# Optimization experiments

Hardware: AMD Instinct MI355X
Metric: run time of the kernel (lower is better)

## Reference

```python
import jax, jax.numpy as jnp
import numpy as np
import math

B, N, IN_DIM, OUT_DIM, H = 8, 1024, 256, 256, 8
D_K = OUT_DIM // H


def setup_inputs() -> dict:
    key = jax.random.key(0)
    ks = jax.random.split(key, 12)
    s_in = 1.0 / math.sqrt(IN_DIM)
    s_out = 1.0 / math.sqrt(OUT_DIM)
    return {
        "X": jax.random.normal(ks[0], (B, N, IN_DIM), jnp.float32),
        "A": jax.random.randint(ks[1], (B, N, N), 0, 2, jnp.int32),
        "D": jax.random.uniform(ks[2], (B, N, N), jnp.float32),
        "W_q": jax.random.uniform(ks[3], (IN_DIM, OUT_DIM), jnp.float32, -s_in, s_in),
        "b_q": jax.random.uniform(ks[4], (OUT_DIM,), jnp.float32, -s_in, s_in),
        "W_k": jax.random.uniform(ks[5], (IN_DIM, OUT_DIM), jnp.float32, -s_in, s_in),
        "b_k": jax.random.uniform(ks[6], (OUT_DIM,), jnp.float32, -s_in, s_in),
        "W_v": jax.random.uniform(ks[7], (IN_DIM, OUT_DIM), jnp.float32, -s_in, s_in),
        "b_v": jax.random.uniform(ks[8], (OUT_DIM,), jnp.float32, -s_in, s_in),
        "W_o": jax.random.uniform(ks[9], (OUT_DIM, OUT_DIM), jnp.float32, -s_out, s_out),
        "b_o": jax.random.uniform(ks[10], (OUT_DIM,), jnp.float32, -s_out, s_out),
        "dist_scale": jnp.array(1.0, jnp.float32),
    }


def reference(X, A, D, W_q, b_q, W_k, b_k, W_v, b_v, W_o, b_o, dist_scale):
    b, n, _ = X.shape
    # Projections -> [B, H, N, d_k]
    Q = (X @ W_q + b_q).reshape(b, n, H, D_K).transpose(0, 2, 1, 3)
    K = (X @ W_k + b_k).reshape(b, n, H, D_K).transpose(0, 2, 1, 3)
    V = (X @ W_v + b_v).reshape(b, n, H, D_K).transpose(0, 2, 1, 3)
    scores = jnp.einsum("bhqd,bhkd->bhqk", Q, K) / jnp.sqrt(jnp.float32(D_K))
    scores = scores - dist_scale * D[:, None, :, :]
    scores = jnp.where(A[:, None, :, :] <= 0, jnp.float32(-1e9), scores)
    attn = jax.nn.softmax(scores, axis=-1)  # dropout is identity in eval mode
    out = jnp.einsum("bhqk,bhkd->bhqd", attn, V)
    out = out.transpose(0, 2, 1, 3).reshape(b, n, H * D_K)
    return out @ W_o + b_o
```

## Files before the change

### kernel.cpp

```cpp
#include <hip/hip_runtime.h>


typedef _Float16 f16x8 __attribute__((ext_vector_type(8)));
typedef __fp16 h16x2 __attribute__((ext_vector_type(2)));
typedef float f32x4 __attribute__((ext_vector_type(4)));
typedef int i32x4 __attribute__((ext_vector_type(4)));
typedef unsigned short u16x8 __attribute__((ext_vector_type(8)));

#define DEV static __device__ __forceinline__

#define LOG2E 1.4426950408889634f
#define QSCALE 0.2550351062f

DEV unsigned short f2h(float f) {
  _Float16 h = (_Float16)f;
  unsigned short u;
  __builtin_memcpy(&u, &h, 2);
  return u;
}

DEV f32x4 mfma16h(f16x8 a, f16x8 b, f32x4 c) {
  return __builtin_amdgcn_mfma_f32_16x16x32_f16(a, b, c, 0, 0, 0);
}

DEV f16x8 ldfragh(const unsigned short* p) {
  return *reinterpret_cast<const f16x8*>(p);
}

__global__ __launch_bounds__(256) void k_prep(
    const float* __restrict__ X, const int* __restrict__ A,
    const float* __restrict__ D, const float* __restrict__ dscale,
    const float* __restrict__ Wq, const float* __restrict__ Wk,
    const float* __restrict__ Wv, const float* __restrict__ Wo,
    unsigned short* __restrict__ Xh, unsigned short* __restrict__ Wt,
    unsigned short* __restrict__ Bias) {
  const int tid = blockIdx.x * 256 + threadIdx.x;
  const int NB4 = (8 * 1024 * 1024) / 4;
  const int NX4 = (8192 * 256) / 4;
  if (tid < NB4) {
    const i32x4 a4 = reinterpret_cast<const i32x4*>(A)[tid];
    const f32x4 d4 = reinterpret_cast<const f32x4*>(D)[tid];
    const float c = -dscale[0] * LOG2E;
    ushort4 o;
    unsigned short* op = (unsigned short*)&o;
    #pragma unroll
    for (int i = 0; i < 4; ++i)
      op[i] = f2h(a4[i] <= 0 ? -60000.0f : c * d4[i]);
    reinterpret_cast<ushort4*>(Bias)[tid] = o;
  } else if (tid < NB4 + NX4) {
    const int t = tid - NB4;
    float4 v = reinterpret_cast<const float4*>(X)[t];
    union { h16x2 h2[2]; ushort4 u; } o;
    o.h2[0] = __builtin_amdgcn_cvt_pkrtz(v.x, v.y);
    o.h2[1] = __builtin_amdgcn_cvt_pkrtz(v.z, v.w);
    reinterpret_cast<ushort4*>(Xh)[t] = o.u;
  } else {
    int t = tid - NB4 - NX4;
    int mat = t >> 16;
    int e = t & 65535;
    int n = e >> 8, k = e & 255;
    const float* W = (mat == 0) ? Wq : (mat == 1) ? Wk : (mat == 2) ? Wv : Wo;
    Wt[t] = f2h(W[k * 256 + n]);
  }
}

__global__ __launch_bounds__(256, 2) void k_qkv(
    const unsigned short* __restrict__ Xh, const unsigned short* __restrict__ Wt,
    const float* __restrict__ bq, const float* __restrict__ bk,
    const float* __restrict__ bv,
    unsigned short* __restrict__ Qb, unsigned short* __restrict__ Kb,
    unsigned short* __restrict__ Vt) {
  const int lane = threadIdx.x & 63;
  const int w = threadIdx.x >> 6;
  const int lr = lane & 15, lg = lane >> 4;
  const int mat = blockIdx.y >> 2;
  const int nloc = (blockIdx.y & 3) * 64 + w * 16;
  const int mbase = blockIdx.x << 8;

  const unsigned short* Wm = Wt + mat * 65536;
  const float* bias = (mat == 0) ? bq : (mat == 1) ? bk : bv;

  f16x8 bfr[8];
  #pragma unroll
  for (int ks = 0; ks < 8; ++ks)
    bfr[ks] = ldfragh(Wm + (nloc + lr) * 256 + ks * 32 + lg * 8);
  const float bb = bias[nloc + lr];
  const int cm = nloc + lr;
  const int hh = cm >> 5, d = cm & 31;

  for (int mt = 0; mt < 16; ++mt) {
    const int m0 = mbase + mt * 16;
    f16x8 a[8];
    #pragma unroll
    for (int ks = 0; ks < 8; ++ks)
      a[ks] = ldfragh(Xh + (m0 + lr) * 256 + ks * 32 + lg * 8);
    f32x4 acc = {0.f, 0.f, 0.f, 0.f};
    #pragma unroll
    for (int ks = 0; ks < 8; ++ks)
      acc = mfma16h(a[ks], bfr[ks], acc);

    if (mat == 2) {
      union { h16x2 h2[2]; ushort4 u; } vv;
      vv.h2[0] = __builtin_amdgcn_cvt_pkrtz(acc[0] + bb, acc[1] + bb);
      vv.h2[1] = __builtin_amdgcn_cvt_pkrtz(acc[2] + bb, acc[3] + bb);
      const int row = m0 + lg * 4;
      const int bidx = row >> 10, nn = row & 1023;
      *reinterpret_cast<ushort4*>(&Vt[(((bidx * 8 + hh) * 32) + d) * 1024 + nn]) = vv.u;
    } else if (mat == 0) {
      #pragma unroll
      for (int i = 0; i < 4; ++i) {
        const int row = m0 + lg * 4 + i;
        const int bidx = row >> 10, nn = row & 1023;
        Qb[(((bidx * 8 + hh) * 1024) + nn) * 32 + d] = f2h((acc[i] + bb) * QSCALE);
      }
    } else {
      #pragma unroll
      for (int i = 0; i < 4; ++i) {
        const int row = m0 + lg * 4 + i;
        const int bidx = row >> 10, nn = row & 1023;
        Kb[(((bidx * 8 + hh) * 1024) + nn) * 32 + d] = f2h(acc[i] + bb);
      }
    }
  }
}

__global__ __launch_bounds__(512, 2) void k_attn(
    const unsigned short* __restrict__ Qb, const unsigned short* __restrict__ Kb,
    const unsigned short* __restrict__ Vt, const unsigned short* __restrict__ Bias,
    unsigned short* __restrict__ AO) {
  __shared__ alignas(16) unsigned short Klds[1024 * 32];
  __shared__ alignas(16) unsigned short Vlds[32 * 1024];
  __shared__ alignas(16) unsigned short Sbuf[8][2][16][40];

  const int tid = threadIdx.x;
  const int lane = tid & 63;
  const int w = tid >> 6;
  const int lr = lane & 15, lg = lane >> 4;
  const int bi = blockIdx.x;
  const int b = bi & 7;
  const int j = bi >> 3;
  const int h = j >> 2, qq = j & 3;
  const int q0w = qq * 256 + w * 32;

  const unsigned short* Kg = Kb + ((size_t)(b * 8 + h) << 15);
  const unsigned short* Vg = Vt + ((size_t)(b * 8 + h) << 15);
  const unsigned short* Qh = Qb + ((size_t)(b * 8 + h) << 15);

  #pragma unroll
  for (int p = 0; p < 8; ++p) {
    const int c = tid + p * 512;
    const int row = c >> 2, seg = c & 3;
    const u16x8 v = *reinterpret_cast<const u16x8*>(Kg + c * 8);
    *reinterpret_cast<u16x8*>(&Klds[row * 32 + ((seg ^ (row & 3)) << 3)]) = v;
  }
  #pragma unroll
  for (int p = 0; p < 8; ++p) {
    const int c = tid + p * 512;
    const int row = c >> 7, ch = c & 127;
    const u16x8 v = *reinterpret_cast<const u16x8*>(Vg + c * 8);
    *reinterpret_cast<u16x8*>(&Vlds[row * 1024 + ((ch ^ (row & 7)) << 3)]) = v;
  }

  f16x8 qf[2];
  qf[0] = ldfragh(Qh + (q0w + lr) * 32 + lg * 8);
  qf[1] = ldfragh(Qh + (q0w + 16 + lr) * 32 + lg * 8);
  const unsigned short* Br0 = Bias + ((size_t)b << 20) + (size_t)(q0w + lr) * 1024;
  const unsigned short* Br1 = Br0 + (size_t)16 * 1024;

  u16x8 bc[2][2], bn[2][2];
  #pragma unroll
  for (int hf = 0; hf < 2; ++hf) {
    bc[0][hf] = *reinterpret_cast<const u16x8*>(Br0 + hf * 32 + lg * 8);
    bc[1][hf] = *reinterpret_cast<const u16x8*>(Br1 + hf * 32 + lg * 8);
  }

  __syncthreads();

  f32x4 o[2][2];
  f32x4 lacc[2];
  #pragma unroll
  for (int s = 0; s < 2; ++s) {
    #pragma unroll
    for (int dh = 0; dh < 2; ++dh) o[s][dh] = f32x4{0.f, 0.f, 0.f, 0.f};
    lacc[s] = f32x4{0.f, 0.f, 0.f, 0.f};
  }
  f16x8 onesv;
  #pragma unroll
  for (int i = 0; i < 8; ++i) onesv[i] = (_Float16)1.0f;

  for (int t = 0; t < 16; ++t) {
    const int k0 = t << 6;
    if (t < 15) {
      #pragma unroll
      for (int hf = 0; hf < 2; ++hf) {
        bn[0][hf] = *reinterpret_cast<const u16x8*>(Br0 + k0 + 64 + hf * 32 + lg * 8);
        bn[1][hf] = *reinterpret_cast<const u16x8*>(Br1 + k0 + 64 + hf * 32 + lg * 8);
      }
    }

    f16x8 kf[4];
    #pragma unroll
    for (int st = 0; st < 4; ++st) {
      const int row = k0 + st * 16 + lr;
      kf[st] = *reinterpret_cast<const f16x8*>(
          &Klds[row * 32 + ((lg ^ (lr & 3)) << 3)]);
    }
    f16x8 vf[2][2];
    #pragma unroll
    for (int dh = 0; dh < 2; ++dh)
      #pragma unroll
      for (int hf = 0; hf < 2; ++hf) {
        const int row = dh * 16 + lr;
        const int ch = t * 8 + ((hf * 4 + lg) ^ (lr & 7));
        vf[dh][hf] = *reinterpret_cast<const f16x8*>(&Vlds[row * 1024 + ch * 8]);
      }

    #pragma unroll
    for (int hf = 0; hf < 2; ++hf) {
      const f32x4 zz = {0.f, 0.f, 0.f, 0.f};
      f32x4 sv[2][2];
      #pragma unroll
      for (int s = 0; s < 2; ++s)
        #pragma unroll
        for (int st = 0; st < 2; ++st)
          sv[s][st] = mfma16h(kf[hf * 2 + st], qf[s], zz);

      #pragma unroll
      for (int s = 0; s < 2; ++s)
        #pragma unroll
        for (int st = 0; st < 2; ++st) {
          union { h16x2 h2[2]; ushort4 u; } sw;
          sw.h2[0] = __builtin_amdgcn_cvt_pkrtz(sv[s][st][0], sv[s][st][1]);
          sw.h2[1] = __builtin_amdgcn_cvt_pkrtz(sv[s][st][2], sv[s][st][3]);
          *reinterpret_cast<ushort4*>(&Sbuf[w][s][lr][st * 16 + lg * 4]) = sw.u;
        }

      #pragma unroll
      for (int s = 0; s < 2; ++s) {
        const f16x8 sf = *reinterpret_cast<const f16x8*>(&Sbuf[w][s][lr][lg * 8]);
        const f16x8 bfv = *reinterpret_cast<const f16x8*>(&bc[s][hf]);
        const f16x8 sb = sf + bfv;
        float e[8];
        #pragma unroll
        for (int i = 0; i < 8; ++i) e[i] = exp2f((float)sb[i]);
        union { h16x2 h2[4]; f16x8 v; } pfu;
        #pragma unroll
        for (int i = 0; i < 4; ++i)
          pfu.h2[i] = __builtin_amdgcn_cvt_pkrtz(e[2 * i], e[2 * i + 1]);
        const f16x8 pf = pfu.v;
        o[s][0] = mfma16h(vf[0][hf], pf, o[s][0]);
        o[s][1] = mfma16h(vf[1][hf], pf, o[s][1]);
        lacc[s] = mfma16h(onesv, pf, lacc[s]);
      }
    }

    #pragma unroll
    for (int s = 0; s < 2; ++s)
      #pragma unroll
      for (int hf = 0; hf < 2; ++hf)
        bc[s][hf] = bn[s][hf];
  }

  #pragma unroll
  for (int s = 0; s < 2; ++s) {
    const float linv = 1.0f / lacc[s][0];
    ushort4 r0, r1;
    unsigned short* r0p = (unsigned short*)&r0;
    unsigned short* r1p = (unsigned short*)&r1;
    #pragma unroll
    for (int i = 0; i < 4; ++i) {
      r0p[i] = f2h(o[s][0][i] * linv);
      r1p[i] = f2h(o[s][1][i] * linv);
    }
    const int row = (b << 10) + q0w + s * 16 + lr;
    *reinterpret_cast<ushort4*>(&AO[row * 256 + h * 32 + lg * 4]) = r0;
    *reinterpret_cast<ushort4*>(&AO[row * 256 + h * 32 + 16 + lg * 4]) = r1;
  }
}

__global__ __launch_bounds__(256, 2) void k_oproj(
    const unsigned short* __restrict__ AO, const unsigned short* __restrict__ Wto,
    const float* __restrict__ bo, float* __restrict__ out) {
  const int lane = threadIdx.x & 63;
  const int w = threadIdx.x >> 6;
  const int lr = lane & 15, lg = lane >> 4;
  const int c0 = blockIdx.y * 64 + w * 16;
  const int mbase = blockIdx.x << 7;

  f16x8 bfr[8];
  #pragma unroll
  for (int ks = 0; ks < 8; ++ks)
    bfr[ks] = ldfragh(Wto + (c0 + lr) * 256 + ks * 32 + lg * 8);
  const float bb = bo[c0 + lr];

  for (int mt = 0; mt < 8; ++mt) {
    const int m0 = mbase + mt * 16;
    f16x8 a[8];
    #pragma unroll
    for (int ks = 0; ks < 8; ++ks)
      a[ks] = ldfragh(AO + (m0 + lr) * 256 + ks * 32 + lg * 8);
    f32x4 acc = {0.f, 0.f, 0.f, 0.f};
    #pragma unroll
    for (int ks = 0; ks < 8; ++ks)
      acc = mfma16h(a[ks], bfr[ks], acc);
    #pragma unroll
    for (int i = 0; i < 4; ++i) {
      const int row = m0 + lg * 4 + i;
      out[row * 256 + c0 + lr] = acc[i] + bb;
    }
  }
}

extern "C" void kernel_launch(void* const* d_in, const int* in_sizes, int n_in,
                              void* d_out, int out_size, void* d_ws, size_t ws_size,
                              hipStream_t stream) {
  const float* X   = (const float*)d_in[0];
  const int*   A   = (const int*)d_in[1];
  const float* D   = (const float*)d_in[2];
  const float* Wq  = (const float*)d_in[3];
  const float* bq  = (const float*)d_in[4];
  const float* Wk  = (const float*)d_in[5];
  const float* bk  = (const float*)d_in[6];
  const float* Wv  = (const float*)d_in[7];
  const float* bv  = (const float*)d_in[8];
  const float* Wo  = (const float*)d_in[9];
  const float* bo  = (const float*)d_in[10];
  const float* dsc = (const float*)d_in[11];
  float* out = (float*)d_out;

  unsigned short* ws = (unsigned short*)d_ws;
  unsigned short* Xh   = ws;
  unsigned short* Wt   = ws + 2097152;
  unsigned short* Qb   = ws + 2359296;
  unsigned short* Kb   = ws + 4456448;
  unsigned short* Vt   = ws + 6553600;
  unsigned short* Bias = ws + 8650752;
  unsigned short* AO   = Xh;

  hipLaunchKernelGGL(k_prep, dim3(11264), dim3(256), 0, stream,
                     X, A, D, dsc, Wq, Wk, Wv, Wo, Xh, Wt, Bias);
  hipLaunchKernelGGL(k_qkv, dim3(32, 12), dim3(256), 0, stream,
                     Xh, Wt, bq, bk, bv, Qb, Kb, Vt);
  hipLaunchKernelGGL(k_attn, dim3(256), dim3(512), 0, stream,
                     Qb, Kb, Vt, Bias, AO);
  hipLaunchKernelGGL(k_oproj, dim3(64, 4), dim3(256), 0, stream,
                     AO, Wt + 196608, bo, out);
}
```

Before: 88.99 us.

## Move bias-mask precompute into QKV projection launch to overlap with GEMM

The A/D to fp16 bias conversion moves out of the prep kernel and into extra blocks appended to the QKV projection kernel, with a flattened 1D grid. The bandwidth-bound bias conversion can then run alongside the compute-bound QKV GEMM blocks instead of before them, and the prep kernel shrinks to converting X and the weights. The cost is mixed block types in one grid, so the heavier GEMM blocks may be scheduled alongside or behind many light bias blocks.

```diff
diff --git a/kernel.cpp b/kernel.cpp
--- a/kernel.cpp
+++ b/kernel.cpp
@@ -27,35 +27,21 @@
   return *reinterpret_cast<const f16x8*>(p);
 }
 
-__global__ __launch_bounds__(256) void k_prep(
-    const float* __restrict__ X, const int* __restrict__ A,
-    const float* __restrict__ D, const float* __restrict__ dscale,
+__global__ __launch_bounds__(256) void k_prep_xw(
+    const float* __restrict__ X,
     const float* __restrict__ Wq, const float* __restrict__ Wk,
     const float* __restrict__ Wv, const float* __restrict__ Wo,
-    unsigned short* __restrict__ Xh, unsigned short* __restrict__ Wt,
-    unsigned short* __restrict__ Bias) {
+    unsigned short* __restrict__ Xh, unsigned short* __restrict__ Wt) {
   const int tid = blockIdx.x * 256 + threadIdx.x;
-  const int NB4 = (8 * 1024 * 1024) / 4;
   const int NX4 = (8192 * 256) / 4;
-  if (tid < NB4) {
-    const i32x4 a4 = reinterpret_cast<const i32x4*>(A)[tid];
-    const f32x4 d4 = reinterpret_cast<const f32x4*>(D)[tid];
-    const float c = -dscale[0] * LOG2E;
-    ushort4 o;
-    unsigned short* op = (unsigned short*)&o;
-    #pragma unroll
-    for (int i = 0; i < 4; ++i)
-      op[i] = f2h(a4[i] <= 0 ? -60000.0f : c * d4[i]);
-    reinterpret_cast<ushort4*>(Bias)[tid] = o;
-  } else if (tid < NB4 + NX4) {
-    const int t = tid - NB4;
-    float4 v = reinterpret_cast<const float4*>(X)[t];
+  if (tid < NX4) {
+    float4 v = reinterpret_cast<const float4*>(X)[tid];
     union { h16x2 h2[2]; ushort4 u; } o;
     o.h2[0] = __builtin_amdgcn_cvt_pkrtz(v.x, v.y);
     o.h2[1] = __builtin_amdgcn_cvt_pkrtz(v.z, v.w);
-    reinterpret_cast<ushort4*>(Xh)[t] = o.u;
+    reinterpret_cast<ushort4*>(Xh)[tid] = o.u;
   } else {
-    int t = tid - NB4 - NX4;
+    int t = tid - NX4;
     int mat = t >> 16;
     int e = t & 65535;
     int n = e >> 8, k = e & 255;
@@ -64,18 +50,35 @@
   }
 }
 
-__global__ __launch_bounds__(256, 2) void k_qkv(
+__global__ __launch_bounds__(256, 2) void k_qkv_bias(
     const unsigned short* __restrict__ Xh, const unsigned short* __restrict__ Wt,
     const float* __restrict__ bq, const float* __restrict__ bk,
     const float* __restrict__ bv,
+    const int* __restrict__ A, const float* __restrict__ D,
+    const float* __restrict__ dscale,
     unsigned short* __restrict__ Qb, unsigned short* __restrict__ Kb,
-    unsigned short* __restrict__ Vt) {
+    unsigned short* __restrict__ Vt, unsigned short* __restrict__ Bias) {
+  if (blockIdx.x >= 384) {
+    const int t = (blockIdx.x - 384) * 256 + threadIdx.x;
+    const i32x4 a4 = reinterpret_cast<const i32x4*>(A)[t];
+    const f32x4 d4 = reinterpret_cast<const f32x4*>(D)[t];
+    const float c = -dscale[0] * LOG2E;
+    ushort4 o;
+    unsigned short* op = (unsigned short*)&o;
+    #pragma unroll
+    for (int i = 0; i < 4; ++i)
+      op[i] = f2h(a4[i] <= 0 ? -60000.0f : c * d4[i]);
+    reinterpret_cast<ushort4*>(Bias)[t] = o;
+    return;
+  }
+
   const int lane = threadIdx.x & 63;
   const int w = threadIdx.x >> 6;
   const int lr = lane & 15, lg = lane >> 4;
-  const int mat = blockIdx.y >> 2;
-  const int nloc = (blockIdx.y & 3) * 64 + w * 16;
-  const int mbase = blockIdx.x << 8;
+  const int yy = blockIdx.x >> 5;
+  const int mat = yy >> 2;
+  const int nloc = (yy & 3) * 64 + w * 16;
+  const int mbase = (blockIdx.x & 31) << 8;
 
   const unsigned short* Wm = Wt + mat * 65536;
   const float* bias = (mat == 0) ? bq : (mat == 1) ? bk : bv;
@@ -337,10 +340,10 @@
   unsigned short* Bias = ws + 8650752;
   unsigned short* AO   = Xh;
 
-  hipLaunchKernelGGL(k_prep, dim3(11264), dim3(256), 0, stream,
-                     X, A, D, dsc, Wq, Wk, Wv, Wo, Xh, Wt, Bias);
-  hipLaunchKernelGGL(k_qkv, dim3(32, 12), dim3(256), 0, stream,
-                     Xh, Wt, bq, bk, bv, Qb, Kb, Vt);
+  hipLaunchKernelGGL(k_prep_xw, dim3(3072), dim3(256), 0, stream,
+                     X, Wq, Wk, Wv, Wo, Xh, Wt);
+  hipLaunchKernelGGL(k_qkv_bias, dim3(8576), dim3(256), 0, stream,
+                     Xh, Wt, bq, bk, bv, A, D, dsc, Qb, Kb, Vt, Bias);
   hipLaunchKernelGGL(k_attn, dim3(256), dim3(512), 0, stream,
                      Qb, Kb, Vt, Bias, AO);
   hipLaunchKernelGGL(k_oproj, dim3(64, 4), dim3(256), 0, stream,
```

Measured after the change: 84.80 us, median of 2. -4.7%, faster.
